# Kernel tuning notes

Measured on AMD Instinct MI355X. Metric: run time of the kernel, lower is better.

Reference implementation:

```python
import jax, jax.numpy as jnp
import numpy as np

B, Q, H, W, C = 2, 8192, 64, 64, 64
C9 = C * 9
EPS = 1e-6


def _mlp(x, params):
    # gelu MLP, no activation on last layer (matches repo mlp)
    for Wm, b in params[:-1]:
        x = jax.nn.gelu(x @ Wm + b)
    Wl, bl = params[-1]
    return x @ Wl + bl


def _make_coord(h, w):
    # pixel-center coords in (-1,1); channel 0 = row dim, channel 1 = col dim
    hs = -1.0 + (2.0 * jnp.arange(h, dtype=jnp.float32) + 1.0) / h
    ws = -1.0 + (2.0 * jnp.arange(w, dtype=jnp.float32) + 1.0) / w
    return jnp.stack(jnp.meshgrid(hs, ws, indexing='ij'), axis=0)  # (2,h,w)


def _nearest_gather(feat, coord):
    # F.grid_sample(mode='nearest', align_corners=False) on a (B,1,q,2) grid.
    # feat (B,C,H,W); coord (B,q,2) with [...,0] indexing H, [...,1] indexing W
    h, w = feat.shape[-2], feat.shape[-1]
    ih = jnp.clip(jnp.round((coord[..., 0] + 1.0) * h / 2.0 - 0.5), 0, h - 1).astype(jnp.int32)
    iw = jnp.clip(jnp.round((coord[..., 1] + 1.0) * w / 2.0 - 0.5), 0, w - 1).astype(jnp.int32)
    return jax.vmap(lambda f, a, b: f[:, a, b].T)(feat, ih, iw)  # (B,q,C)


def _unfold3(feat):
    # F.unfold(feat, 3, padding=1).view(B, C*9, H, W): channel-major, kernel row-major
    b, c, h, w = feat.shape
    p = jnp.pad(feat, ((0, 0), (0, 0), (1, 1), (1, 1)))
    patches = jnp.stack([p[:, :, i:i + h, j:j + w] for i in range(3) for j in range(3)], axis=2)
    return patches.reshape(b, c * 9, h, w)


def _forward(inp, coord, scale, enc_w, enc_b, iw0, ib0, iw1, ib1, iw2, ib2,
             sw0, sb0, sw1, sb1, ww0, wb0, ww1, wb1):
    # encoder (stand-in conv3x3, 3 -> C feature channels)
    feat = jax.lax.conv_general_dilated(inp, enc_w, (1, 1), 'SAME',
                                        dimension_numbers=('NCHW', 'OIHW', 'NCHW'))
    feat = feat + enc_b[None, :, None, None]
    feat = _unfold3(feat)  # (B, C*9, H, W)
    bsz, cf, h, w = feat.shape
    fcoord = jnp.broadcast_to(_make_coord(h, w)[None], (bsz, 2, h, w))
    dims = jnp.array([h, w], dtype=feat.dtype)

    tx = (h - 1) / (1.0 - scale[:, 0, 0])  # (B,)
    ty = (w - 1) / (1.0 - scale[:, 0, 1])
    rx, ry = 1.0 / tx, 1.0 / ty
    scale_tok = scale * dims  # (B,q,2)

    imnet_p = [(iw0, ib0), (iw1, ib1), (iw2, ib2)]
    score_p = [(sw0, sb0), (sw1, sb1)]
    weight_p = [(ww0, wb0), (ww1, wb1)]

    preds = []
    for vx in (-1, 1):
        for vy in (-1, 1):
            shift = jnp.stack([vx * rx + EPS, vy * ry + EPS], axis=-1)[:, None, :]  # (B,1,2)
            c = jnp.clip(coord + shift, -1.0 + 1e-6, 1.0 - 1e-6)
            value = _nearest_gather(feat, c)      # (B,q,C*9)
            coord_k = _nearest_gather(fcoord, c)  # (B,q,2)
            rel = (coord - coord_k) * dims        # (B,q,2)
            score = _mlp(rel, score_p)            # (B,q,1) -> broadcast over 3
            mlp_in = jnp.concatenate([rel, scale_tok], axis=-1)  # (B,q,4)
            wmat = _mlp(mlp_in, imnet_p).reshape(bsz, -1, cf, 3)  # (B,q,C*9,3)
            preds.append(jnp.einsum('bqc,bqck->bqk', value, wmat) + score)
    stacked = jnp.stack(preds, axis=-1)  # (B,q,3,4)
    return _mlp(stacked, weight_p)[..., 0]  # (B,q,3)


def setup_inputs() -> dict:
    key = jax.random.key(0)
    ks = jax.random.split(key, 16)
    f32 = jnp.float32

    def wi(k, shape, fan_in):
        return jax.random.normal(k, shape, f32) / np.float32(np.sqrt(fan_in))

    return {
        'inp': jax.random.normal(ks[0], (B, 3, H, W), f32),
        'coord': jax.random.uniform(ks[1], (B, Q, 2), f32, -1.0 + 1e-4, 1.0 - 1e-4),
        'scale': jax.random.uniform(ks[2], (B, Q, 2), f32, 0.01, 0.05),
        'enc_w': wi(ks[3], (C, 3, 3, 3), 27),
        'enc_b': jnp.zeros((C,), f32),
        'iw0': wi(ks[4], (4, 256), 4), 'ib0': jnp.zeros((256,), f32),
        'iw1': wi(ks[5], (256, 256), 256), 'ib1': jnp.zeros((256,), f32),
        'iw2': wi(ks[6], (256, C9 * 3), 256), 'ib2': jnp.zeros((C9 * 3,), f32),
        'sw0': wi(ks[7], (2, 256), 2), 'sb0': jnp.zeros((256,), f32),
        'sw1': wi(ks[8], (256, 1), 256), 'sb1': jnp.zeros((1,), f32),
        'ww0': wi(ks[9], (4, 256), 4), 'wb0': jnp.zeros((256,), f32),
        'ww1': wi(ks[10], (256, 1), 256), 'wb1': jnp.zeros((1,), f32),
    }


def reference(inp, coord, scale, enc_w, enc_b, iw0, ib0, iw1, ib1, iw2, ib2,
              sw0, sb0, sw1, sb1, ww0, wb0, ww1, wb1):
    return _forward(inp, coord, scale, enc_w, enc_b, iw0, ib0, iw1, ib1, iw2, ib2,
                    sw0, sb0, sw1, sb1, ww0, wb0, ww1, wb1)
```

## Files before the change

### kernel.cpp

```cpp
#include <hip/hip_runtime.h>

#define QN 8192
#define CCH 64
#define NROW 65536
#define MR 64
#define NBLK (NROW / MR)
#define H0S 264

typedef _Float16 f16x8 __attribute__((ext_vector_type(8)));
typedef _Float16 f16x4 __attribute__((ext_vector_type(4)));
typedef float f32x4 __attribute__((ext_vector_type(4)));

__device__ __forceinline__ float gelu_f(float x) {
    float x2 = x * x;
    float tt = fmaf(0.044715f, x2, 1.0f);
    float e = __expf(1.5957691216f * x * tt);
    float r = __builtin_amdgcn_rcpf(1.0f + e);
    return x - x * r;
}

__global__ __launch_bounds__(256) void k_pre(const float* __restrict__ inp,
                                             const float* __restrict__ ew,
                                             const float* __restrict__ eb,
                                             const float* __restrict__ coord,
                                             const float* __restrict__ scale,
                                             const float* __restrict__ sw0,
                                             const float* __restrict__ sb0,
                                             const float* __restrict__ sw1,
                                             const float* __restrict__ sb1,
                                             const float* __restrict__ iw1,
                                             const float* __restrict__ iw2,
                                             const float* __restrict__ ib2,
                                             float* __restrict__ featpad,
                                             float4* __restrict__ mlp_in,
                                             int2* __restrict__ ihiw,
                                             float* __restrict__ scoreg,
                                             _Float16* __restrict__ w1tp,
                                             _Float16* __restrict__ w2tp,
                                             float* __restrict__ b2p) {
    const int bb = blockIdx.x;
    const int tt0 = threadIdx.x;
    if (bb < 2178) {
        __shared__ float s_ew[1728];
        for (int i = tt0; i < 1728; i += 256) s_ew[i] = ew[i];
        __syncthreads();
        int idx = bb * 256 + tt0;
        const int total = 2 * 66 * 66 * CCH;
        if (idx >= total) return;
        int o = idx & 63; int pix = idx >> 6;
        int xx = pix % 66; int t2 = pix / 66;
        int yy = t2 % 66;  int b = t2 / 66;
        int y = yy - 1, x = xx - 1;
        float acc = 0.0f;
        if (y >= 0 && y < 64 && x >= 0 && x < 64) {
            acc = eb[o];
            for (int i = 0; i < 3; ++i) {
                const float* ip = inp + ((b * 3 + i) * 64) * 64;
                const float* wp = s_ew + (o * 3 + i) * 9;
                #pragma unroll
                for (int ky = 0; ky < 3; ++ky) {
                    int sy = y + ky - 1;
                    if (sy < 0 || sy > 63) continue;
                    #pragma unroll
                    for (int kx = 0; kx < 3; ++kx) {
                        int sx = x + kx - 1;
                        if (sx < 0 || sx > 63) continue;
                        acc += ip[sy * 64 + sx] * wp[ky * 3 + kx];
                    }
                }
            }
        }
        featpad[idx] = acc;
    } else if (bb < 2434) {
        int row = (bb - 2178) * 256 + tt0;
        int v = row & 3;
        int bq = row >> 2;
        int b = bq >> 13;
        float c0 = coord[bq * 2 + 0], c1 = coord[bq * 2 + 1];
        float s0 = scale[bq * 2 + 0], s1 = scale[bq * 2 + 1];
        float s00 = scale[(b * QN) * 2 + 0];
        float s01 = scale[(b * QN) * 2 + 1];
        float rx = (1.0f - s00) / 63.0f;
        float ry = (1.0f - s01) / 63.0f;
        float vx = (v & 2) ? 1.0f : -1.0f;
        float vy = (v & 1) ? 1.0f : -1.0f;
        float cc0 = c0 + vx * rx + 1e-6f;
        float cc1 = c1 + vy * ry + 1e-6f;
        cc0 = fminf(fmaxf(cc0, -1.0f + 1e-6f), 1.0f - 1e-6f);
        cc1 = fminf(fmaxf(cc1, -1.0f + 1e-6f), 1.0f - 1e-6f);
        int ih = (int)rintf((cc0 + 1.0f) * 32.0f - 0.5f);
        int iw = (int)rintf((cc1 + 1.0f) * 32.0f - 0.5f);
        ih = min(max(ih, 0), 63);
        iw = min(max(iw, 0), 63);
        float ck0 = (2.0f * (float)ih + 1.0f) / 64.0f - 1.0f;
        float ck1 = (2.0f * (float)iw + 1.0f) / 64.0f - 1.0f;
        float rel0 = (c0 - ck0) * 64.0f;
        float rel1 = (c1 - ck1) * 64.0f;
        mlp_in[row] = make_float4(rel0, rel1, s0 * 64.0f, s1 * 64.0f);
        ihiw[row] = make_int2(ih, iw);
        float sc = sb1[0];
        #pragma unroll 4
        for (int t2 = 0; t2 < 256; ++t2) {
            float h = gelu_f(fmaf(rel0, sw0[t2], fmaf(rel1, sw0[256 + t2], sb0[t2])));
            sc = fmaf(h, sw1[t2], sc);
        }
        scoreg[row] = sc;
    } else {
        int idx = (bb - 2434) * 256 + tt0;
        if (idx < 442368) {
            int j = idx & 7, ln = (idx >> 3) & 63, kf = (idx >> 9) & 7, tl = idx >> 12;
            int np = tl * 16 + (ln & 15);
            int kk = kf * 32 + (ln >> 4) * 8 + j;
            int k_out = np / 576;
            int rem = np - 576 * k_out;
            int tap = rem >> 6, cch = rem & 63;
            int n = (cch * 9 + tap) * 3 + k_out;
            w2tp[idx] = (_Float16)iw2[kk * 1728 + n];
            if (kf == 0 && j == 0 && (ln >> 4) == 0) b2p[np] = ib2[n];
        } else {
            int i2 = idx - 442368;
            int j = i2 & 7, ln = (i2 >> 3) & 63, kf = (i2 >> 9) & 7, ct = i2 >> 12;
            int col = ct * 16 + (ln & 15);
            int kk = kf * 32 + (ln >> 4) * 8 + j;
            w1tp[i2] = (_Float16)iw1[kk * 256 + col];
        }
    }
}

__global__ __launch_bounds__(256, 2) void k_fused(const float* __restrict__ featpad,
                                                  const float4* __restrict__ mlp_in,
                                                  const int2* __restrict__ ihiw,
                                                  const float* __restrict__ iw0,
                                                  const float* __restrict__ ib0,
                                                  const _Float16* __restrict__ w1tp,
                                                  const float* __restrict__ ib1,
                                                  const _Float16* __restrict__ w2tp,
                                                  const float* __restrict__ b2p,
                                                  const float* __restrict__ scoreg,
                                                  const float* __restrict__ ww0,
                                                  const float* __restrict__ wb0,
                                                  const float* __restrict__ ww1,
                                                  const float* __restrict__ wb1,
                                                  float* __restrict__ out) {
    __shared__ __align__(16) char pool[576 * 64 * 2];
    _Float16* s_h0   = (_Float16*)pool;
    _Float16* s_valT = (_Float16*)pool;
    __shared__ float4 s_min[MR];
    __shared__ int    s_base[MR];
    __shared__ int    s_dtab[9];
    __shared__ float  s_pred[MR][3];
    __shared__ float  s_score[MR];
    __shared__ float  s_wred[48][4];

    const int t = threadIdx.x;
    const int wave = t >> 6, lane = t & 63, quad = lane >> 4, l15 = lane & 15;
    const int rowbase = blockIdx.x * MR;

    if (t < MR) {
        int row = rowbase + t;
        s_min[t] = mlp_in[row];
        s_score[t] = scoreg[row];
        int b = row >> 15;
        int2 p = ihiw[row];
        s_base[t] = ((b * 66 + p.x) * 66 + p.y) * 64;
    }
    if (t < 9) { int di = t / 3; s_dtab[t] = (di * 66 + (t - 3 * di)) * 64; }
    if (t < MR * 3) s_pred[t / 3][t % 3] = 0.0f;
    __syncthreads();

    {
        float w0 = iw0[t], w1 = iw0[256 + t], w2 = iw0[512 + t], w3 = iw0[768 + t];
        float bb = ib0[t];
        #pragma unroll 4
        for (int r = 0; r < MR; ++r) {
            float4 m = s_min[r];
            s_h0[r * H0S + t] =
                (_Float16)gelu_f(fmaf(m.x, w0, fmaf(m.y, w1, fmaf(m.z, w2, fmaf(m.w, w3, bb)))));
        }
    }
    __syncthreads();

    f16x8 a[4][8];
    #pragma unroll
    for (int rt = 0; rt < 4; ++rt)
        #pragma unroll
        for (int kf = 0; kf < 8; ++kf)
            a[rt][kf] = *(const f16x8*)(s_h0 + (rt * 16 + l15) * H0S + kf * 32 + quad * 8);
    __syncthreads();

    #pragma unroll 1
    for (int c = 0; c < 4; ++c) {
        int ct = wave * 4 + c;
        f16x8 bf[8];
        #pragma unroll
        for (int kf = 0; kf < 8; ++kf)
            bf[kf] = *(const f16x8*)(w1tp + ((ct * 8 + kf) * 64 + lane) * 8);
        f32x4 acc[4] = {{0.f,0.f,0.f,0.f},{0.f,0.f,0.f,0.f},{0.f,0.f,0.f,0.f},{0.f,0.f,0.f,0.f}};
        #pragma unroll
        for (int kf = 0; kf < 8; ++kf)
            #pragma unroll
            for (int rt = 0; rt < 4; ++rt)
                acc[rt] = __builtin_amdgcn_mfma_f32_16x16x32_f16(a[rt][kf], bf[kf], acc[rt], 0, 0, 0);
        int col = ct * 16 + l15;
        float bias = ib1[col];
        #pragma unroll
        for (int rt = 0; rt < 4; ++rt)
            #pragma unroll
            for (int reg = 0; reg < 4; ++reg)
                s_h0[(rt * 16 + quad * 4 + reg) * H0S + col] = (_Float16)gelu_f(acc[rt][reg] + bias);
    }
    __syncthreads();

    #pragma unroll
    for (int rt = 0; rt < 4; ++rt)
        #pragma unroll
        for (int kf = 0; kf < 8; ++kf)
            a[rt][kf] = *(const f16x8*)(s_h0 + (rt * 16 + l15) * H0S + kf * 32 + quad * 8);
    __syncthreads();

    const int tbase = wave * 27;
    f16x8 bfX[4], bfY[4];
    {
        const _Float16* wp = w2tp + (size_t)(tbase * 8) * 512 + lane * 8;
        #pragma unroll
        for (int kf = 0; kf < 4; ++kf) bfX[kf] = *(const f16x8*)(wp + kf * 512);
    }

    #pragma unroll 1
    for (int it = 0; it < 36; ++it) {
        int p = (wave * 36 + it) * 4 + quad;
        int r = (p * 7283) >> 16;
        int tap = p - 9 * r;
        const float4 v = *(const float4*)(featpad + s_base[r] + s_dtab[tap] + l15 * 4);
        int cfp0 = tap * 64 + l15 * 4;
        int g = (cfp0 & 15) << 2;
        _Float16* wp = s_valT + cfp0 * 64 + (r ^ ((cfp0 & 12) << 2));
        s_valT[(cfp0 + 0) * 64 + (r ^ (((cfp0 + 0) & 15) << 2))] = (_Float16)v.x;
        s_valT[(cfp0 + 1) * 64 + (r ^ (((cfp0 + 1) & 15) << 2))] = (_Float16)v.y;
        s_valT[(cfp0 + 2) * 64 + (r ^ (((cfp0 + 2) & 15) << 2))] = (_Float16)v.z;
        s_valT[(cfp0 + 3) * 64 + (r ^ (((cfp0 + 3) & 15) << 2))] = (_Float16)v.w;
        (void)g; (void)wp;
    }
    __syncthreads();

    const int kt0 = tbase / 36;
    int bsplit = (kt0 + 1) * 36 - tbase; if (bsplit > 27) bsplit = 27;
    const int ktB = (tbase + 26) / 36;

    float pA[4][4];
    #pragma unroll
    for (int rt = 0; rt < 4; ++rt)
        #pragma unroll
        for (int rg = 0; rg < 4; ++rg) pA[rt][rg] = 0.f;

    float bv;
    #pragma unroll 1
    for (int i = 0; i < 27; ++i) {
        int ti = tbase + i;
        {
            const _Float16* wp = w2tp + (size_t)(ti * 8 + 4) * 512 + lane * 8;
            #pragma unroll
            for (int kf = 0; kf < 4; ++kf) bfY[kf] = *(const f16x8*)(wp + kf * 512);
            bv = b2p[ti * 16 + l15];
        }
        f32x4 acc[4] = {{0.f,0.f,0.f,0.f},{0.f,0.f,0.f,0.f},{0.f,0.f,0.f,0.f},{0.f,0.f,0.f,0.f}};
        #pragma unroll
        for (int kf = 0; kf < 4; ++kf)
            #pragma unroll
            for (int rt = 0; rt < 4; ++rt)
                acc[rt] = __builtin_amdgcn_mfma_f32_16x16x32_f16(a[rt][kf], bfX[kf], acc[rt], 0, 0, 0);
        if (i < 26) {
            const _Float16* wp = w2tp + (size_t)((ti + 1) * 8) * 512 + lane * 8;
            #pragma unroll
            for (int kf = 0; kf < 4; ++kf) bfX[kf] = *(const f16x8*)(wp + kf * 512);
        }
        #pragma unroll
        for (int kf = 0; kf < 4; ++kf)
            #pragma unroll
            for (int rt = 0; rt < 4; ++rt)
                acc[rt] = __builtin_amdgcn_mfma_f32_16x16x32_f16(a[rt][kf + 4], bfY[kf], acc[rt], 0, 0, 0);
        int cf36 = ti - (ti / 36) * 36;
        int cfp = cf36 * 16 + l15;
        int g = (cfp & 15) << 2;
        const _Float16* vbase = s_valT + cfp * 64;
        #pragma unroll
        for (int rt = 0; rt < 4; ++rt) {
            f16x4 vv = *(const f16x4*)(vbase + ((rt * 16 + quad * 4) ^ g));
            #pragma unroll
            for (int rg = 0; rg < 4; ++rg) {
                float s = acc[rt][rg] + bv;
                pA[rt][rg] = fmaf(s, (float)vv[rg], pA[rt][rg]);
            }
        }
        if (i == bsplit - 1) {
            #pragma unroll
            for (int rt = 0; rt < 4; ++rt)
                #pragma unroll
                for (int rg = 0; rg < 4; ++rg) {
                    float x = pA[rt][rg];
                    #pragma unroll
                    for (int m = 1; m < 16; m <<= 1) x += __shfl_xor(x, m, 64);
                    if (l15 == 0) atomicAdd(&s_pred[rt * 16 + quad * 4 + rg][kt0], x);
                    pA[rt][rg] = 0.f;
                }
        }
    }
    #pragma unroll
    for (int rt = 0; rt < 4; ++rt)
        #pragma unroll
        for (int rg = 0; rg < 4; ++rg) {
            float x = pA[rt][rg];
            #pragma unroll
            for (int m = 1; m < 16; m <<= 1) x += __shfl_xor(x, m, 64);
            if (l15 == 0) atomicAdd(&s_pred[rt * 16 + quad * 4 + rg][ktB], x);
        }
    __syncthreads();

    if (t < 192) {
        int o = t >> 2, sub = t & 3;
        int bql = o / 3, k = o - 3 * bql;
        float x0 = s_pred[bql * 4 + 0][k] + s_score[bql * 4 + 0];
        float x1 = s_pred[bql * 4 + 1][k] + s_score[bql * 4 + 1];
        float x2 = s_pred[bql * 4 + 2][k] + s_score[bql * 4 + 2];
        float x3 = s_pred[bql * 4 + 3][k] + s_score[bql * 4 + 3];
        float acc = 0.0f;
        int j0 = sub * 64;
        #pragma unroll 4
        for (int j = j0; j < j0 + 64; ++j) {
            float h = gelu_f(fmaf(x0, ww0[j], fmaf(x1, ww0[256 + j],
                          fmaf(x2, ww0[512 + j], fmaf(x3, ww0[768 + j], wb0[j])))));
            acc = fmaf(h, ww1[j], acc);
        }
        s_wred[o][sub] = acc;
    }
    __syncthreads();
    if (t < 48) {
        int bql = t / 3, k = t - 3 * bql;
        float r2 = s_wred[t][0] + s_wred[t][1] + s_wred[t][2] + s_wred[t][3] + wb1[0];
        out[(blockIdx.x * 16 + bql) * 3 + k] = r2;
    }
}

extern "C" void kernel_launch(void* const* d_in, const int* in_sizes, int n_in,
                              void* d_out, int out_size, void* d_ws, size_t ws_size,
                              hipStream_t stream) {
    const float* inp   = (const float*)d_in[0];
    const float* coord = (const float*)d_in[1];
    const float* scale = (const float*)d_in[2];
    const float* ew    = (const float*)d_in[3];
    const float* eb    = (const float*)d_in[4];
    const float* iw0   = (const float*)d_in[5];
    const float* ib0   = (const float*)d_in[6];
    const float* iw1   = (const float*)d_in[7];
    const float* ib1   = (const float*)d_in[8];
    const float* iw2   = (const float*)d_in[9];
    const float* ib2   = (const float*)d_in[10];
    const float* sw0   = (const float*)d_in[11];
    const float* sb0   = (const float*)d_in[12];
    const float* sw1   = (const float*)d_in[13];
    const float* sb1   = (const float*)d_in[14];
    const float* ww0   = (const float*)d_in[15];
    const float* wb0   = (const float*)d_in[16];
    const float* ww1   = (const float*)d_in[17];
    const float* wb1   = (const float*)d_in[18];
    float* out = (float*)d_out;

    char* ws = (char*)d_ws;
    float*     featpad = (float*)(ws + 0);
    float4*    mlp_in  = (float4*)(ws + 2230272);
    int2*      ihiw    = (int2*)(ws + 3278848);
    float*     scoreg  = (float*)(ws + 3803136);
    _Float16*  w1tp    = (_Float16*)(ws + 4065280);
    _Float16*  w2tp    = (_Float16*)(ws + 4196352);
    float*     b2p     = (float*)(ws + 5081088);

    k_pre<<<dim3(4418), dim3(256), 0, stream>>>(inp, ew, eb, coord, scale,
                                                sw0, sb0, sw1, sb1, iw1, iw2, ib2,
                                                featpad, mlp_in, ihiw, scoreg,
                                                w1tp, w2tp, b2p);
    k_fused<<<dim3(NBLK), dim3(256), 0, stream>>>(featpad, mlp_in, ihiw,
                                                  iw0, ib0, w1tp, ib1, w2tp, b2p,
                                                  scoreg, ww0, wb0, ww1, wb1, out);
}
```

Before: 251.2 us.

## Double-buffer layer-1 weight loads and restructure feature gather with new LDS swizzle

The hidden-layer MFMA loop now loads its B-fragments in two halves, prefetching the next column tile's first half while the current second half computes, so global load latency overlaps with MFMA work. The unfolded-feature gather is also reorganized: each lane handles one row, and every wave issues four float4 loads before writing them to shared memory. The LDS transpose swizzle changes from a 4-element to an 8-element XOR pattern, and the consumer read is updated to match. This should reduce load stalls and LDS bank conflicts, at the cost of more live registers.

```diff
diff --git a/kernel.cpp b/kernel.cpp
--- a/kernel.cpp
+++ b/kernel.cpp
@@ -180,6 +180,13 @@
     }
     __syncthreads();
 
+    f16x8 hX[4], hY[4];
+    {
+        const _Float16* wp = w1tp + (size_t)((wave * 4) * 8) * 512 + lane * 8;
+        #pragma unroll
+        for (int kf = 0; kf < 4; ++kf) hX[kf] = *(const f16x8*)(wp + kf * 512);
+    }
+
     f16x8 a[4][8];
     #pragma unroll
     for (int rt = 0; rt < 4; ++rt)
@@ -191,16 +198,27 @@
     #pragma unroll 1
     for (int c = 0; c < 4; ++c) {
         int ct = wave * 4 + c;
-        f16x8 bf[8];
-        #pragma unroll
-        for (int kf = 0; kf < 8; ++kf)
-            bf[kf] = *(const f16x8*)(w1tp + ((ct * 8 + kf) * 64 + lane) * 8);
+        {
+            const _Float16* wp = w1tp + (size_t)(ct * 8 + 4) * 512 + lane * 8;
+            #pragma unroll
+            for (int kf = 0; kf < 4; ++kf) hY[kf] = *(const f16x8*)(wp + kf * 512);
+        }
         f32x4 acc[4] = {{0.f,0.f,0.f,0.f},{0.f,0.f,0.f,0.f},{0.f,0.f,0.f,0.f},{0.f,0.f,0.f,0.f}};
         #pragma unroll
-        for (int kf = 0; kf < 8; ++kf)
+        for (int kf = 0; kf < 4; ++kf)
             #pragma unroll
             for (int rt = 0; rt < 4; ++rt)
-                acc[rt] = __builtin_amdgcn_mfma_f32_16x16x32_f16(a[rt][kf], bf[kf], acc[rt], 0, 0, 0);
+                acc[rt] = __builtin_amdgcn_mfma_f32_16x16x32_f16(a[rt][kf], hX[kf], acc[rt], 0, 0, 0);
+        if (c < 3) {
+            const _Float16* wp = w1tp + (size_t)((ct + 1) * 8) * 512 + lane * 8;
+            #pragma unroll
+            for (int kf = 0; kf < 4; ++kf) hX[kf] = *(const f16x8*)(wp + kf * 512);
+        }
+        #pragma unroll
+        for (int kf = 0; kf < 4; ++kf)
+            #pragma unroll
+            for (int rt = 0; rt < 4; ++rt)
+                acc[rt] = __builtin_amdgcn_mfma_f32_16x16x32_f16(a[rt][kf + 4], hY[kf], acc[rt], 0, 0, 0);
         int col = ct * 16 + l15;
         float bias = ib1[col];
         #pragma unroll
@@ -227,25 +245,31 @@
     }
 
     #pragma unroll 1
-    for (int it = 0; it < 36; ++it) {
-        int p = (wave * 36 + it) * 4 + quad;
-        int r = (p * 7283) >> 16;
-        int tap = p - 9 * r;
-        const float4 v = *(const float4*)(featpad + s_base[r] + s_dtab[tap] + l15 * 4);
-        int cfp0 = tap * 64 + l15 * 4;
-        int g = (cfp0 & 15) << 2;
-        _Float16* wp = s_valT + cfp0 * 64 + (r ^ ((cfp0 & 12) << 2));
-        s_valT[(cfp0 + 0) * 64 + (r ^ (((cfp0 + 0) & 15) << 2))] = (_Float16)v.x;
-        s_valT[(cfp0 + 1) * 64 + (r ^ (((cfp0 + 1) & 15) << 2))] = (_Float16)v.y;
-        s_valT[(cfp0 + 2) * 64 + (r ^ (((cfp0 + 2) & 15) << 2))] = (_Float16)v.z;
-        s_valT[(cfp0 + 3) * 64 + (r ^ (((cfp0 + 3) & 15) << 2))] = (_Float16)v.w;
-        (void)g; (void)wp;
+    for (int g4 = 0; g4 < 9; ++g4) {
+        float4 v[4];
+        #pragma unroll
+        for (int u = 0; u < 4; ++u) {
+            int c4 = wave + (g4 * 4 + u) * 4;
+            int tap = c4 >> 4;
+            int cch0 = (c4 & 15) << 2;
+            v[u] = *(const float4*)(featpad + s_base[lane] + s_dtab[tap] + cch0);
+        }
+        #pragma unroll
+        for (int u = 0; u < 4; ++u) {
+            int c4 = wave + (g4 * 4 + u) * 4;
+            int cfp = c4 << 2;
+            s_valT[(cfp + 0) * 64 + (lane ^ (((cfp + 0) & 7) << 3))] = (_Float16)v[u].x;
+            s_valT[(cfp + 1) * 64 + (lane ^ (((cfp + 1) & 7) << 3))] = (_Float16)v[u].y;
+            s_valT[(cfp + 2) * 64 + (lane ^ (((cfp + 2) & 7) << 3))] = (_Float16)v[u].z;
+            s_valT[(cfp + 3) * 64 + (lane ^ (((cfp + 3) & 7) << 3))] = (_Float16)v[u].w;
+        }
     }
     __syncthreads();
 
     const int kt0 = tbase / 36;
     int bsplit = (kt0 + 1) * 36 - tbase; if (bsplit > 27) bsplit = 27;
     const int ktB = (tbase + 26) / 36;
+    const int swz = (l15 & 7) << 3;
 
     float pA[4][4];
     #pragma unroll
@@ -281,11 +305,10 @@
                 acc[rt] = __builtin_amdgcn_mfma_f32_16x16x32_f16(a[rt][kf + 4], bfY[kf], acc[rt], 0, 0, 0);
         int cf36 = ti - (ti / 36) * 36;
         int cfp = cf36 * 16 + l15;
-        int g = (cfp & 15) << 2;
         const _Float16* vbase = s_valT + cfp * 64;
         #pragma unroll
         for (int rt = 0; rt < 4; ++rt) {
-            f16x4 vv = *(const f16x4*)(vbase + ((rt * 16 + quad * 4) ^ g));
+            f16x4 vv = *(const f16x4*)(vbase + ((rt * 16 + quad * 4) ^ swz));
             #pragma unroll
             for (int rg = 0; rg < 4; ++rg) {
                 float s = acc[rt][rg] + bv;
```

Result: faster. 240.4 us (-4.3%).
